# Optimization experiments

Hardware: AMD Instinct MI355X
Metric: run time of the kernel (lower is better)

Reference implementation:

```python
import jax, jax.numpy as jnp
import numpy as np

C, H, V, K, B, T = 1024, 256, 10000, 32, 8, 256
K1K = 2 * K + 1


def setup_inputs() -> dict:
    key = jax.random.key(0)
    ks = jax.random.split(key, 12)
    s = 0.05
    n = lambda k, shp: jax.random.normal(k, shp, dtype=jnp.float32) * s
    z = lambda shp: jnp.zeros(shp, dtype=jnp.float32)
    return {
        'text': jax.random.randint(ks[0], (B, T), 0, V, dtype=jnp.int32),
        'start_emb': n(ks[1], (H,)),
        'start_lin_W': n(ks[2], (H, H)), 'start_lin_b': z((H,)),
        'start_res_W1': n(ks[3], (2, H, H)), 'start_res_b1': z((2, H)),
        'start_res_W2': n(ks[4], (2, H, H)), 'start_res_b2': z((2, H)),
        'state_emb': n(ks[5], (C, H)),
        'next_state_emb': n(ks[6], (C, H)),
        'preterminal_emb': n(ks[7], (C, H)),
        'term_res_W1': n(ks[8], (2, H, H)), 'term_res_b1': z((2, H)),
        'term_res_W2': n(ks[9], (2, H, H)), 'term_res_b2': z((2, H)),
        'terminal_emb': n(ks[10], (V, H)),
        'col_banded_transition': n(ks[11], (C, K1K)),
    }


def _res(x, W1, b1, W2, b2):
    # ResLayer: x + ReLU(Linear(ReLU(Linear(x))))
    h = jax.nn.relu(x @ W1.T + b1)
    h = jax.nn.relu(h @ W2.T + b2)
    return x + h


def _band_to_dense(band):
    # BandedMatrix(band[None], K, K, fill=0).to_dense(): dense[i, i+d] = band[i, d+K] for |d|<=K
    offs = jnp.arange(-K, K + 1)                  # (K1K,)
    rows = jnp.arange(C)
    cols = rows[:, None] + offs[None, :]          # (C, K1K)
    valid = (cols >= 0) & (cols < C)
    vals = jnp.where(valid, band, 0.0)
    return jnp.zeros((C, C), band.dtype).at[rows[:, None], jnp.clip(cols, 0, C - 1)].add(vals)


def reference(text, start_emb, start_lin_W, start_lin_b,
              start_res_W1, start_res_b1, start_res_W2, start_res_b2,
              state_emb, next_state_emb, preterminal_emb,
              term_res_W1, term_res_b1, term_res_W2, term_res_b2,
              terminal_emb, col_banded_transition):
    # start(): MLP(start_emb) @ next_state_emb.T (tie_start), log_softmax -> (C,)
    fx = start_emb @ start_lin_W.T + start_lin_b
    for i in range(2):
        fx = _res(fx, start_res_W1[i], start_res_b1[i], start_res_W2[i], start_res_b2[i])
    start = jax.nn.log_softmax(fx @ next_state_emb.T)

    # transition(): dense logits + banded logits (band_method='product'), row log_softmax -> (C, C)
    logits = state_emb @ next_state_emb.T
    trans = jax.nn.log_softmax(logits + _band_to_dense(col_banded_transition), axis=-1)

    # emission(): terminal_mlp(preterminal_emb) @ terminal_emb.T, log_softmax -> (C, V)
    ft = preterminal_emb
    for i in range(2):
        ft = _res(ft, term_res_W1[i], term_res_b1[i], term_res_W2[i], term_res_b2[i])
    emit_T = jax.nn.log_softmax(ft @ terminal_emb.T, axis=-1).T  # (V, C)

    # HMM forward algorithm over time (log semiring)
    alpha = start[None, :] + emit_T[text[:, 0]]  # (B, C)

    def step(alpha, toks):
        # alpha_next[b, j] = logsumexp_i(alpha[b, i] + trans[i, j]) + emit[j, tok_b]
        a = jax.nn.logsumexp(alpha[:, :, None] + trans[None], axis=1) + emit_T[toks]
        return a, None

    alpha, _ = jax.lax.scan(step, alpha, text[:, 1:].T)
    return jax.nn.logsumexp(alpha, axis=-1)  # (B,) log-evidence
```

## Files before the change

### kernel.cpp

```cpp
#include <hip/hip_runtime.h>

constexpr int C = 1024, H = 256, V = 10000, K = 32, B = 8, T = 256, K1K = 65;
constexpr int DB = 32;
constexpr int GSCAN = B * DB;
constexpr float LV = 9.210340371976184f;

#define DEV static __device__ __forceinline__

typedef float f4 __attribute__((ext_vector_type(4)));

DEV void gstore(float* p, float v) {
  __hip_atomic_store((unsigned*)p, __float_as_uint(v), __ATOMIC_RELAXED, __HIP_MEMORY_SCOPE_AGENT);
}
DEV float gload(const float* p) {
  return __uint_as_float(__hip_atomic_load((unsigned*)p, __ATOMIC_RELAXED, __HIP_MEMORY_SCOPE_AGENT));
}
DEV void fstore(unsigned* p, unsigned v) {
  __hip_atomic_store(p, v, __ATOMIC_RELAXED, __HIP_MEMORY_SCOPE_AGENT);
}
DEV unsigned fload(const unsigned* p) {
  return __hip_atomic_load(p, __ATOMIC_RELAXED, __HIP_MEMORY_SCOPE_AGENT);
}

__global__ void __launch_bounds__(256) k_pre(
    const float* __restrict__ semb, const float* __restrict__ linW, const float* __restrict__ linb,
    const float* __restrict__ srW1, const float* __restrict__ srb1,
    const float* __restrict__ srW2, const float* __restrict__ srb2,
    const float* __restrict__ nse, const float* __restrict__ se,
    const float* __restrict__ pre, const float* __restrict__ trW1, const float* __restrict__ trb1,
    const float* __restrict__ trW2, const float* __restrict__ trb2,
    const float* __restrict__ band,
    unsigned* __restrict__ flags, float* __restrict__ startv,
    float* __restrict__ ft, float* __restrict__ PT) {
  __shared__ float smem[2048];
  const int bid = blockIdx.x, tid = threadIdx.x;

  if (bid == 0) {
    for (int k = tid; k < B * DB * 16; k += 256) flags[k] = 0u;
    return;
  }

  if (bid == 1) {
    float* sa = smem;
    float* fx = smem + 256;
    float* hh = smem + 512;
    float* sl = smem + 768;
    float* red = smem + 1792;
    sa[tid] = semb[tid];
    __syncthreads();
    float acc = linb[tid];
    for (int h = 0; h < H; ++h) acc += sa[h] * linW[tid * H + h];
    fx[tid] = acc;
    __syncthreads();
    for (int l = 0; l < 2; ++l) {
      float a1 = srb1[l * H + tid];
      const float* w1 = srW1 + (size_t)l * H * H + (size_t)tid * H;
      for (int h = 0; h < H; ++h) a1 += fx[h] * w1[h];
      hh[tid] = fmaxf(a1, 0.f);
      __syncthreads();
      float a2 = srb2[l * H + tid];
      const float* w2 = srW2 + (size_t)l * H * H + (size_t)tid * H;
      for (int h = 0; h < H; ++h) a2 += hh[h] * w2[h];
      __syncthreads();
      fx[tid] += fmaxf(a2, 0.f);
      __syncthreads();
    }
    for (int q = 0; q < 4; ++q) {
      int c = q * 256 + tid;
      const float* nr = nse + (size_t)c * H;
      float s = 0.f;
      for (int h = 0; h < H; ++h) s += fx[h] * nr[h];
      sl[c] = s;
    }
    __syncthreads();
    float m = -__builtin_inff();
    for (int q = 0; q < 4; ++q) m = fmaxf(m, sl[q * 256 + tid]);
    red[tid] = m; __syncthreads();
    for (int off = 128; off > 0; off >>= 1) { if (tid < off) red[tid] = fmaxf(red[tid], red[tid + off]); __syncthreads(); }
    m = red[0]; __syncthreads();
    float s = 0.f;
    for (int q = 0; q < 4; ++q) s += __expf(sl[q * 256 + tid] - m);
    red[tid] = s; __syncthreads();
    for (int off = 128; off > 0; off >>= 1) { if (tid < off) red[tid] += red[tid + off]; __syncthreads(); }
    float lse = m + __logf(red[0]);
    for (int q = 0; q < 4; ++q) { int c = q * 256 + tid; startv[c] = sl[c] - lse; }
    return;
  }

  if (bid < 258) {
    float (*x)[H] = (float(*)[H])smem;
    float (*hh)[H] = (float(*)[H])(smem + 1024);
    int r0 = (bid - 2) * 4;
    for (int r = 0; r < 4; ++r) x[r][tid] = pre[(size_t)(r0 + r) * H + tid];
    __syncthreads();
    for (int l = 0; l < 2; ++l) {
      float bb = trb1[l * H + tid];
      float a0 = bb, a1 = bb, a2 = bb, a3 = bb;
      const float* w1 = trW1 + (size_t)l * H * H + (size_t)tid * H;
      for (int h = 0; h < H; ++h) {
        float w = w1[h];
        a0 += x[0][h] * w; a1 += x[1][h] * w; a2 += x[2][h] * w; a3 += x[3][h] * w;
      }
      hh[0][tid] = fmaxf(a0, 0.f); hh[1][tid] = fmaxf(a1, 0.f);
      hh[2][tid] = fmaxf(a2, 0.f); hh[3][tid] = fmaxf(a3, 0.f);
      __syncthreads();
      bb = trb2[l * H + tid];
      float b0 = bb, b1 = bb, b2 = bb, b3 = bb;
      const float* w2 = trW2 + (size_t)l * H * H + (size_t)tid * H;
      for (int h = 0; h < H; ++h) {
        float w = w2[h];
        b0 += hh[0][h] * w; b1 += hh[1][h] * w; b2 += hh[2][h] * w; b3 += hh[3][h] * w;
      }
      __syncthreads();
      x[0][tid] += fmaxf(b0, 0.f); x[1][tid] += fmaxf(b1, 0.f);
      x[2][tid] += fmaxf(b2, 0.f); x[3][tid] += fmaxf(b3, 0.f);
      __syncthreads();
    }
    for (int r = 0; r < 4; ++r) ft[(size_t)(r0 + r) * H + tid] = x[r][tid];
    return;
  }

  {
    float* sv = smem;
    float* sl = smem + 256;
    float* rr = smem + 1280;
    int i = bid - 258;
    sv[tid] = se[(size_t)i * H + tid];
    __syncthreads();
    #pragma unroll 1
    for (int jq = 0; jq < 4; ++jq) {
      int j = jq * 256 + tid;
      const float4* nr = (const float4*)(nse + (size_t)j * H);
      float acc = 0.f;
      #pragma unroll 8
      for (int h4 = 0; h4 < H / 4; ++h4) {
        float4 nv = nr[h4];
        float4 s4 = *(const float4*)&sv[h4 * 4];
        acc += s4.x * nv.x + s4.y * nv.y + s4.z * nv.z + s4.w * nv.w;
      }
      sl[j] = acc;
    }
    __syncthreads();
    if (tid < K1K) {
      int col = i + tid - K;
      if (col >= 0 && col < C) sl[col] += band[(size_t)i * K1K + tid];
    }
    __syncthreads();
    float m = -__builtin_inff();
    for (int q = 0; q < 4; ++q) m = fmaxf(m, sl[q * 256 + tid]);
    rr[tid] = m; __syncthreads();
    for (int off = 128; off > 0; off >>= 1) { if (tid < off) rr[tid] = fmaxf(rr[tid], rr[tid + off]); __syncthreads(); }
    m = rr[0]; __syncthreads();
    float e[4]; float s = 0.f;
    for (int q = 0; q < 4; ++q) { e[q] = __expf(sl[q * 256 + tid] - m); s += e[q]; }
    rr[tid] = s; __syncthreads();
    for (int off = 128; off > 0; off >>= 1) { if (tid < off) rr[tid] += rr[tid + off]; __syncthreads(); }
    float inv = 1.f / rr[0];
    for (int q = 0; q < 4; ++q) {
      int j = q * 256 + tid;
      PT[(size_t)j * C + i] = e[q] * inv;
    }
  }
}

__global__ void __launch_bounds__(256) k_denom_part(
    const float* __restrict__ ft, const float* __restrict__ term, float* __restrict__ dpart) {
  constexpr int TJ = 16, VC = V / 8;
  __shared__ float shm[TJ * 4], shs[TJ * 4];
  int tid = threadIdx.x, lane = tid & 63, w = tid >> 6;
  int jg = blockIdx.x >> 3, vc = blockIdx.x & 7;
  const float4* fb = (const float4*)(ft + (size_t)jg * TJ * H);
  float rm[TJ], rs[TJ];
  #pragma unroll
  for (int r = 0; r < TJ; ++r) { rm[r] = -__builtin_inff(); rs[r] = 0.f; }
  int v0 = vc * VC;
  for (int v = v0 + tid; v < v0 + VC; v += 256) {
    const float4* tr = (const float4*)(term + (size_t)v * H);
    float acc[TJ];
    #pragma unroll
    for (int r = 0; r < TJ; ++r) acc[r] = 0.f;
    for (int h4 = 0; h4 < H / 4; ++h4) {
      float4 tv = tr[h4];
      #pragma unroll
      for (int r = 0; r < TJ; ++r) {
        float4 f = fb[r * (H / 4) + h4];
        acc[r] += tv.x * f.x + tv.y * f.y + tv.z * f.z + tv.w * f.w;
      }
    }
    #pragma unroll
    for (int r = 0; r < TJ; ++r) {
      float m2 = fmaxf(rm[r], acc[r]);
      rs[r] = rs[r] * __expf(rm[r] - m2) + __expf(acc[r] - m2);
      rm[r] = m2;
    }
  }
  #pragma unroll
  for (int r = 0; r < TJ; ++r) {
    float m = rm[r], s = rs[r];
    #pragma unroll
    for (int off = 32; off > 0; off >>= 1) {
      float mo = __shfl_xor(m, off), so = __shfl_xor(s, off);
      float m2 = fmaxf(m, mo);
      s = s * __expf(m - m2) + so * __expf(mo - m2);
      m = m2;
    }
    if (lane == 0) { shm[r * 4 + w] = m; shs[r * 4 + w] = s; }
  }
  __syncthreads();
  if (tid < TJ) {
    float m = -__builtin_inff(), s = 0.f;
    for (int w2 = 0; w2 < 4; ++w2) {
      float mo = shm[tid * 4 + w2], so = shs[tid * 4 + w2];
      float m2 = fmaxf(m, mo);
      s = s * __expf(m - m2) + so * __expf(mo - m2);
      m = m2;
    }
    int j = jg * TJ + tid;
    dpart[(j * 8 + vc) * 2 + 0] = m;
    dpart[(j * 8 + vc) * 2 + 1] = s;
  }
}

__global__ void k_denom_comb(const float* __restrict__ dpart, float* __restrict__ denom) {
  int j = blockIdx.x * 256 + threadIdx.x;
  float m = -__builtin_inff(), s = 0.f;
  for (int vc = 0; vc < 8; ++vc) {
    float mo = dpart[(j * 8 + vc) * 2], so = dpart[(j * 8 + vc) * 2 + 1];
    float m2 = fmaxf(m, mo);
    s = s * __expf(m - m2) + so * __expf(mo - m2);
    m = m2;
  }
  denom[j] = m + __logf(s);
}

__global__ void __launch_bounds__(256) k_eemit(
    const int* __restrict__ text, const float* __restrict__ ft,
    const float* __restrict__ denom, const float* __restrict__ term,
    float* __restrict__ eem) {
  int tid = threadIdx.x;
  int n0 = blockIdx.x * 8;
  const float4* trow[8];
  #pragma unroll
  for (int r = 0; r < 8; ++r) {
    int n = n0 + r;
    int tok = text[(n & 7) * T + (n >> 3)];
    trow[r] = (const float4*)(term + (size_t)tok * H);
  }
  for (int q = 0; q < 4; ++q) {
    int j = q * 256 + tid;
    const float4* fr = (const float4*)(ft + (size_t)j * H);
    float acc[8];
    #pragma unroll
    for (int r = 0; r < 8; ++r) acc[r] = 0.f;
    for (int h4 = 0; h4 < H / 4; ++h4) {
      float4 f = fr[h4];
      #pragma unroll
      for (int r = 0; r < 8; ++r) {
        float4 tv = trow[r][h4];
        acc[r] += f.x * tv.x + f.y * tv.y + f.z * tv.z + f.w * tv.w;
      }
    }
    float dj = denom[j];
    #pragma unroll
    for (int r = 0; r < 8; ++r) eem[(size_t)(n0 + r) * C + j] = __expf(acc[r] - dj + LV);
  }
}

__global__ void __launch_bounds__(256, 1) k_scan(
    const float* __restrict__ PT, const float* __restrict__ eem,
    const float* __restrict__ startv, float* __restrict__ pay,
    float* __restrict__ umax, unsigned* __restrict__ flags, float* __restrict__ out) {
  __shared__ __align__(16) float us[8 * 132];
  __shared__ float wv[32];
  __shared__ float fred[256];
  const int tid = threadIdx.x, bid = blockIdx.x;
  const int b = bid & 7, blk = bid >> 3;
  const int jbase = blk * 32;
  const int jloc = tid >> 3, s = tid & 7;
  const int myj = jbase + jloc;
  const bool owner = (s == 0);

  f4 pv[32];
  {
    const f4* prow = (const f4*)(PT + (size_t)myj * C + s * 128);
    #pragma unroll
    for (int k4 = 0; k4 < 32; ++k4) pv[k4] = prow[k4];
  }

  unsigned* myflag = &flags[(b * DB + blk) * 16];
  float Sacc = 0.f;

  if (owner) {
    float u0 = __expf(startv[myj]) * eem[(size_t)b * C + myj];
    gstore(&pay[(size_t)b * (DB * DB) + blk * DB + jloc], u0);
  }
  __syncthreads();
  if (tid == 0) fstore(myflag, 1u);

  float em = 0.f;
  if (owner) em = eem[((size_t)1 * B + b) * C + myj];

  for (int t = 1; t < T; ++t) {
    if (tid < DB) {
      while (fload(&flags[(b * DB + tid) * 16]) < (unsigned)t) {}
    }
    __syncthreads();

    float imt = 1.f;
    if (owner && (t & 7) == 1 && t > 1) {
      float m = gload(&umax[((t - 1) >> 3) * 8 + b]);
      imt = 1.f / m;
      Sacc += __logf(m);
    }

    {
      int i = (tid >> 3) * 32 + (tid & 7) * 4;
      const float* src = pay + (size_t)(((t - 1) & 1) * 8 + b) * (DB * DB) + i;
      f4 r;
      asm volatile("global_load_dwordx4 %0, %1, off sc0 sc1\n\ts_waitcnt vmcnt(0)"
                   : "=v"(r) : "v"(src) : "memory");
      int ph = (i >> 7) * 132 + (i & 127);
      *(f4*)&us[ph] = r;
    }
    __syncthreads();

    float acc = 0.f;
    {
      const int ubo = s * 132;
      #pragma unroll
      for (int k4 = 0; k4 < 32; ++k4) {
        f4 p = pv[k4];
        f4 x = *(const f4*)&us[ubo + k4 * 4];
        acc += p.x * x.x + p.y * x.y + p.z * x.z + p.w * x.w;
      }
    }
    acc += __shfl_xor(acc, 1);
    acc += __shfl_xor(acc, 2);
    acc += __shfl_xor(acc, 4);

    if (owner) {
      float val = acc * imt * em;
      gstore(&pay[(size_t)((t & 1) * 8 + b) * (DB * DB) + blk * DB + jloc], val);
      if (blk == 0) wv[jloc] = val;
    }
    __syncthreads();

    if (blk == 0 && (t & 7) == 0 && tid == 0) {
      float m = wv[0];
      #pragma unroll
      for (int j2 = 1; j2 < 32; ++j2) m = fmaxf(m, wv[j2]);
      gstore(&umax[(t >> 3) * 8 + b], m);
      asm volatile("s_waitcnt vmcnt(0)" ::: "memory");
    }
    if (tid == 0) fstore(myflag, (unsigned)(t + 1));
    if (owner && t + 1 < T) em = eem[((size_t)(t + 1) * B + b) * C + myj];
  }

  if (tid < DB) {
    while (fload(&flags[(b * DB + tid) * 16]) < (unsigned)T) {}
  }
  __syncthreads();
  if (blk == 0) {
    {
      int i = (tid >> 3) * 32 + (tid & 7) * 4;
      const float* src = pay + (size_t)(((T - 1) & 1) * 8 + b) * (DB * DB) + i;
      f4 r;
      asm volatile("global_load_dwordx4 %0, %1, off sc0 sc1\n\ts_waitcnt vmcnt(0)"
                   : "=v"(r) : "v"(src) : "memory");
      int ph = (i >> 7) * 132 + (i & 127);
      *(f4*)&us[ph] = r;
    }
    __syncthreads();
    float ss = 0.f;
    for (int idx = tid; idx < C; idx += 256) ss += us[(idx >> 7) * 132 + (idx & 127)];
    fred[tid] = ss;
    __syncthreads();
    for (int off = 128; off > 0; off >>= 1) {
      if (tid < off) fred[tid] += fred[tid + off];
      __syncthreads();
    }
    if (tid == 0) out[b] = -(float)T * LV + Sacc + __logf(fred[0]);
  }
}

extern "C" void kernel_launch(void* const* d_in, const int* in_sizes, int n_in,
                              void* d_out, int out_size, void* d_ws, size_t ws_size,
                              hipStream_t stream) {
  const int*   text  = (const int*)  d_in[0];
  const float* semb  = (const float*)d_in[1];
  const float* slinW = (const float*)d_in[2];
  const float* slinb = (const float*)d_in[3];
  const float* srW1  = (const float*)d_in[4];
  const float* srb1  = (const float*)d_in[5];
  const float* srW2  = (const float*)d_in[6];
  const float* srb2  = (const float*)d_in[7];
  const float* stemb = (const float*)d_in[8];
  const float* nse   = (const float*)d_in[9];
  const float* pre   = (const float*)d_in[10];
  const float* trW1  = (const float*)d_in[11];
  const float* trb1  = (const float*)d_in[12];
  const float* trW2  = (const float*)d_in[13];
  const float* trb2  = (const float*)d_in[14];
  const float* term  = (const float*)d_in[15];
  const float* band  = (const float*)d_in[16];

  float* ws     = (float*)d_ws;
  float* PT     = ws;
  float* eem    = PT + (size_t)C * C;
  float* pay    = eem + (size_t)T * B * C;
  float* ftb    = pay + 2 * 8 * DB * DB;
  float* startv = ftb + (size_t)C * H;
  float* denom  = startv + C;
  float* dpart  = denom + C;
  float* umax   = dpart + C * 16;
  unsigned* flags = (unsigned*)(umax + 32 * 8);

  k_pre<<<1282, 256, 0, stream>>>(semb, slinW, slinb, srW1, srb1, srW2, srb2,
                                  nse, stemb, pre, trW1, trb1, trW2, trb2, band,
                                  flags, startv, ftb, PT);
  k_denom_part<<<(C / 16) * 8, 256, 0, stream>>>(ftb, term, dpart);
  k_denom_comb<<<C / 256, 256, 0, stream>>>(dpart, denom);
  k_eemit<<<(T * B) / 8, 256, 0, stream>>>(text, ftb, denom, term, eem);
  k_scan<<<GSCAN, 256, 0, stream>>>(PT, eem, startv, pay, umax, flags, (float*)d_out);
}
```

Baseline: 969.4 us.

## Replace flag-based scan sync with sentinel-tagged payload polling and tune pre kernels

The cross-block HMM scan stops spinning on per-block flag counters. Each consumer now polls the payload buffer directly, which is 4-deep and pre-filled with a negative-sign sentinel, and producers reset slots two steps ahead. This removes a flag round-trip and one barrier per time step, at the risk of relying on alpha values never having the sign bit set. The terminal MLP inner loops are also vectorised with float4 accumulators, and the denominator kernel's row tile is doubled to 32.

```diff
diff --git a/kernel.cpp b/kernel.cpp
--- a/kernel.cpp
+++ b/kernel.cpp
@@ -4,6 +4,7 @@
 constexpr int DB = 32;
 constexpr int GSCAN = B * DB;
 constexpr float LV = 9.210340371976184f;
+constexpr unsigned SENT = 0x80000000u;
 
 #define DEV static __device__ __forceinline__
 
@@ -14,12 +15,6 @@
 }
 DEV float gload(const float* p) {
   return __uint_as_float(__hip_atomic_load((unsigned*)p, __ATOMIC_RELAXED, __HIP_MEMORY_SCOPE_AGENT));
-}
-DEV void fstore(unsigned* p, unsigned v) {
-  __hip_atomic_store(p, v, __ATOMIC_RELAXED, __HIP_MEMORY_SCOPE_AGENT);
-}
-DEV unsigned fload(const unsigned* p) {
-  return __hip_atomic_load(p, __ATOMIC_RELAXED, __HIP_MEMORY_SCOPE_AGENT);
 }
 
 __global__ void __launch_bounds__(256) k_pre(
@@ -30,17 +25,19 @@
     const float* __restrict__ pre, const float* __restrict__ trW1, const float* __restrict__ trb1,
     const float* __restrict__ trW2, const float* __restrict__ trb2,
     const float* __restrict__ band,
-    unsigned* __restrict__ flags, float* __restrict__ startv,
+    float* __restrict__ pay, float* __restrict__ startv,
     float* __restrict__ ft, float* __restrict__ PT) {
   __shared__ float smem[2048];
   const int bid = blockIdx.x, tid = threadIdx.x;
 
-  if (bid == 0) {
-    for (int k = tid; k < B * DB * 16; k += 256) flags[k] = 0u;
+  if (bid < 16) {
+    unsigned* p = (unsigned*)pay;
+    #pragma unroll
+    for (int k = 0; k < 8; ++k) p[bid * 2048 + k * 256 + tid] = SENT;
     return;
   }
 
-  if (bid == 1) {
+  if (bid == 16) {
     float* sa = smem;
     float* fx = smem + 256;
     float* hh = smem + 512;
@@ -87,33 +84,49 @@
     return;
   }
 
-  if (bid < 258) {
+  if (bid < 273) {
     float (*x)[H] = (float(*)[H])smem;
     float (*hh)[H] = (float(*)[H])(smem + 1024);
-    int r0 = (bid - 2) * 4;
+    int r0 = (bid - 17) * 4;
     for (int r = 0; r < 4; ++r) x[r][tid] = pre[(size_t)(r0 + r) * H + tid];
     __syncthreads();
     for (int l = 0; l < 2; ++l) {
-      float bb = trb1[l * H + tid];
-      float a0 = bb, a1 = bb, a2 = bb, a3 = bb;
-      const float* w1 = trW1 + (size_t)l * H * H + (size_t)tid * H;
-      for (int h = 0; h < H; ++h) {
-        float w = w1[h];
-        a0 += x[0][h] * w; a1 += x[1][h] * w; a2 += x[2][h] * w; a3 += x[3][h] * w;
-      }
-      hh[0][tid] = fmaxf(a0, 0.f); hh[1][tid] = fmaxf(a1, 0.f);
-      hh[2][tid] = fmaxf(a2, 0.f); hh[3][tid] = fmaxf(a3, 0.f);
-      __syncthreads();
-      bb = trb2[l * H + tid];
-      float b0 = bb, b1 = bb, b2 = bb, b3 = bb;
-      const float* w2 = trW2 + (size_t)l * H * H + (size_t)tid * H;
-      for (int h = 0; h < H; ++h) {
-        float w = w2[h];
-        b0 += hh[0][h] * w; b1 += hh[1][h] * w; b2 += hh[2][h] * w; b3 += hh[3][h] * w;
-      }
-      __syncthreads();
-      x[0][tid] += fmaxf(b0, 0.f); x[1][tid] += fmaxf(b1, 0.f);
-      x[2][tid] += fmaxf(b2, 0.f); x[3][tid] += fmaxf(b3, 0.f);
+      {
+        const f4* w1 = (const f4*)(trW1 + (size_t)l * H * H + (size_t)tid * H);
+        f4 p0 = {0.f, 0.f, 0.f, 0.f}, p1 = p0, p2 = p0, p3 = p0;
+        #pragma unroll 8
+        for (int h4 = 0; h4 < H / 4; ++h4) {
+          f4 w = w1[h4];
+          p0 += w * *(const f4*)&x[0][h4 * 4];
+          p1 += w * *(const f4*)&x[1][h4 * 4];
+          p2 += w * *(const f4*)&x[2][h4 * 4];
+          p3 += w * *(const f4*)&x[3][h4 * 4];
+        }
+        float bb = trb1[l * H + tid];
+        hh[0][tid] = fmaxf(p0.x + p0.y + p0.z + p0.w + bb, 0.f);
+        hh[1][tid] = fmaxf(p1.x + p1.y + p1.z + p1.w + bb, 0.f);
+        hh[2][tid] = fmaxf(p2.x + p2.y + p2.z + p2.w + bb, 0.f);
+        hh[3][tid] = fmaxf(p3.x + p3.y + p3.z + p3.w + bb, 0.f);
+      }
+      __syncthreads();
+      {
+        const f4* w2 = (const f4*)(trW2 + (size_t)l * H * H + (size_t)tid * H);
+        f4 q0 = {0.f, 0.f, 0.f, 0.f}, q1 = q0, q2 = q0, q3 = q0;
+        #pragma unroll 8
+        for (int h4 = 0; h4 < H / 4; ++h4) {
+          f4 w = w2[h4];
+          q0 += w * *(const f4*)&hh[0][h4 * 4];
+          q1 += w * *(const f4*)&hh[1][h4 * 4];
+          q2 += w * *(const f4*)&hh[2][h4 * 4];
+          q3 += w * *(const f4*)&hh[3][h4 * 4];
+        }
+        float bb = trb2[l * H + tid];
+        __syncthreads();
+        x[0][tid] += fmaxf(q0.x + q0.y + q0.z + q0.w + bb, 0.f);
+        x[1][tid] += fmaxf(q1.x + q1.y + q1.z + q1.w + bb, 0.f);
+        x[2][tid] += fmaxf(q2.x + q2.y + q2.z + q2.w + bb, 0.f);
+        x[3][tid] += fmaxf(q3.x + q3.y + q3.z + q3.w + bb, 0.f);
+      }
       __syncthreads();
     }
     for (int r = 0; r < 4; ++r) ft[(size_t)(r0 + r) * H + tid] = x[r][tid];
@@ -124,7 +137,7 @@
     float* sv = smem;
     float* sl = smem + 256;
     float* rr = smem + 1280;
-    int i = bid - 258;
+    int i = bid - 273;
     sv[tid] = se[(size_t)i * H + tid];
     __syncthreads();
     #pragma unroll 1
@@ -165,7 +178,7 @@
 
 __global__ void __launch_bounds__(256) k_denom_part(
     const float* __restrict__ ft, const float* __restrict__ term, float* __restrict__ dpart) {
-  constexpr int TJ = 16, VC = V / 8;
+  constexpr int TJ = 32, VC = V / 8;
   __shared__ float shm[TJ * 4], shs[TJ * 4];
   int tid = threadIdx.x, lane = tid & 63, w = tid >> 6;
   int jg = blockIdx.x >> 3, vc = blockIdx.x & 7;
@@ -269,15 +282,14 @@
 __global__ void __launch_bounds__(256, 1) k_scan(
     const float* __restrict__ PT, const float* __restrict__ eem,
     const float* __restrict__ startv, float* __restrict__ pay,
-    float* __restrict__ umax, unsigned* __restrict__ flags, float* __restrict__ out) {
+    float* __restrict__ umax, float* __restrict__ out) {
   __shared__ __align__(16) float us[8 * 132];
   __shared__ float wv[32];
   __shared__ float fred[256];
   const int tid = threadIdx.x, bid = blockIdx.x;
   const int b = bid & 7, blk = bid >> 3;
-  const int jbase = blk * 32;
   const int jloc = tid >> 3, s = tid & 7;
-  const int myj = jbase + jloc;
+  const int myj = blk * 32 + jloc;
   const bool owner = (s == 0);
 
   f4 pv[32];
@@ -285,26 +297,42 @@
     const f4* prow = (const f4*)(PT + (size_t)myj * C + s * 128);
     #pragma unroll
     for (int k4 = 0; k4 < 32; ++k4) pv[k4] = prow[k4];
-  }
-
-  unsigned* myflag = &flags[(b * DB + blk) * 16];
+    #pragma unroll
+    for (int k4 = 0; k4 < 32; ++k4) asm volatile("" : "+v"(pv[k4]));
+  }
+
   float Sacc = 0.f;
 
   if (owner) {
     float u0 = __expf(startv[myj]) * eem[(size_t)b * C + myj];
-    gstore(&pay[(size_t)b * (DB * DB) + blk * DB + jloc], u0);
-  }
-  __syncthreads();
-  if (tid == 0) fstore(myflag, 1u);
-
-  float em = 0.f;
-  if (owner) em = eem[((size_t)1 * B + b) * C + myj];
-
+    gstore(&pay[(size_t)b * C + myj], u0);
+  }
+  float em = owner ? eem[((size_t)B + b) * C + myj] : 0.f;
+
+  const int pi = tid * 4;
   for (int t = 1; t < T; ++t) {
-    if (tid < DB) {
-      while (fload(&flags[(b * DB + tid) * 16]) < (unsigned)t) {}
-    }
-    __syncthreads();
+    {
+      const float* src = pay + (size_t)((t - 1) & 3) * (B * C) + (size_t)b * C + pi;
+      f4 r;
+      for (;;) {
+        asm volatile("global_load_dwordx4 %0, %1, off sc0 sc1\n\ts_waitcnt vmcnt(0)"
+                     : "=v"(r) : "v"(src) : "memory");
+        unsigned bits = __float_as_uint(r.x) | __float_as_uint(r.y) |
+                        __float_as_uint(r.z) | __float_as_uint(r.w);
+        if (!(bits & 0x80000000u)) break;
+        __builtin_amdgcn_s_sleep(1);
+      }
+      int ph = (pi >> 7) * 132 + (pi & 127);
+      *(f4*)&us[ph] = r;
+    }
+    __syncthreads();
+
+    if (tid < 8) {
+      float* dst = pay + (size_t)((t + 1) & 3) * (B * C) + (size_t)b * C + blk * 32 + tid * 4;
+      f4 sn;
+      sn.x = sn.y = sn.z = sn.w = __uint_as_float(SENT);
+      asm volatile("global_store_dwordx4 %0, %1, off sc0 sc1" :: "v"(dst), "v"(sn) : "memory");
+    }
 
     float imt = 1.f;
     if (owner && (t & 7) == 1 && t > 1) {
@@ -312,17 +340,6 @@
       imt = 1.f / m;
       Sacc += __logf(m);
     }
-
-    {
-      int i = (tid >> 3) * 32 + (tid & 7) * 4;
-      const float* src = pay + (size_t)(((t - 1) & 1) * 8 + b) * (DB * DB) + i;
-      f4 r;
-      asm volatile("global_load_dwordx4 %0, %1, off sc0 sc1\n\ts_waitcnt vmcnt(0)"
-                   : "=v"(r) : "v"(src) : "memory");
-      int ph = (i >> 7) * 132 + (i & 127);
-      *(f4*)&us[ph] = r;
-    }
-    __syncthreads();
 
     float acc = 0.f;
     {
@@ -338,11 +355,12 @@
     acc += __shfl_xor(acc, 2);
     acc += __shfl_xor(acc, 4);
 
+    float val = 0.f;
     if (owner) {
-      float val = acc * imt * em;
-      gstore(&pay[(size_t)((t & 1) * 8 + b) * (DB * DB) + blk * DB + jloc], val);
+      val = acc * imt * em;
       if (blk == 0) wv[jloc] = val;
     }
+    if (tid < 8) asm volatile("s_waitcnt vmcnt(0)" ::: "memory");
     __syncthreads();
 
     if (blk == 0 && (t & 7) == 0 && tid == 0) {
@@ -352,28 +370,24 @@
       gstore(&umax[(t >> 3) * 8 + b], m);
       asm volatile("s_waitcnt vmcnt(0)" ::: "memory");
     }
-    if (tid == 0) fstore(myflag, (unsigned)(t + 1));
+    if (owner) gstore(&pay[(size_t)(t & 3) * (B * C) + (size_t)b * C + myj], val);
     if (owner && t + 1 < T) em = eem[((size_t)(t + 1) * B + b) * C + myj];
   }
 
-  if (tid < DB) {
-    while (fload(&flags[(b * DB + tid) * 16]) < (unsigned)T) {}
-  }
-  __syncthreads();
   if (blk == 0) {
     {
-      int i = (tid >> 3) * 32 + (tid & 7) * 4;
-      const float* src = pay + (size_t)(((T - 1) & 1) * 8 + b) * (DB * DB) + i;
+      const float* src = pay + (size_t)((T - 1) & 3) * (B * C) + (size_t)b * C + pi;
       f4 r;
-      asm volatile("global_load_dwordx4 %0, %1, off sc0 sc1\n\ts_waitcnt vmcnt(0)"
-                   : "=v"(r) : "v"(src) : "memory");
-      int ph = (i >> 7) * 132 + (i & 127);
-      *(f4*)&us[ph] = r;
-    }
-    __syncthreads();
-    float ss = 0.f;
-    for (int idx = tid; idx < C; idx += 256) ss += us[(idx >> 7) * 132 + (idx & 127)];
-    fred[tid] = ss;
+      for (;;) {
+        asm volatile("global_load_dwordx4 %0, %1, off sc0 sc1\n\ts_waitcnt vmcnt(0)"
+                     : "=v"(r) : "v"(src) : "memory");
+        unsigned bits = __float_as_uint(r.x) | __float_as_uint(r.y) |
+                        __float_as_uint(r.z) | __float_as_uint(r.w);
+        if (!(bits & 0x80000000u)) break;
+        __builtin_amdgcn_s_sleep(1);
+      }
+      fred[tid] = r.x + r.y + r.z + r.w;
+    }
     __syncthreads();
     for (int off = 128; off > 0; off >>= 1) {
       if (tid < off) fred[tid] += fred[tid + off];
@@ -408,18 +422,17 @@
   float* PT     = ws;
   float* eem    = PT + (size_t)C * C;
   float* pay    = eem + (size_t)T * B * C;
-  float* ftb    = pay + 2 * 8 * DB * DB;
+  float* ftb    = pay + 4 * B * C;
   float* startv = ftb + (size_t)C * H;
   float* denom  = startv + C;
   float* dpart  = denom + C;
   float* umax   = dpart + C * 16;
-  unsigned* flags = (unsigned*)(umax + 32 * 8);
-
-  k_pre<<<1282, 256, 0, stream>>>(semb, slinW, slinb, srW1, srb1, srW2, srb2,
+
+  k_pre<<<1297, 256, 0, stream>>>(semb, slinW, slinb, srW1, srb1, srW2, srb2,
                                   nse, stemb, pre, trW1, trb1, trW2, trb2, band,
-                                  flags, startv, ftb, PT);
-  k_denom_part<<<(C / 16) * 8, 256, 0, stream>>>(ftb, term, dpart);
+                                  pay, startv, ftb, PT);
+  k_denom_part<<<(C / 32) * 8, 256, 0, stream>>>(ftb, term, dpart);
   k_denom_comb<<<C / 256, 256, 0, stream>>>(dpart, denom);
   k_eemit<<<(T * B) / 8, 256, 0, stream>>>(text, ftb, denom, term, eem);
-  k_scan<<<GSCAN, 256, 0, stream>>>(PT, eem, startv, pay, umax, flags, (float*)d_out);
-}
+  k_scan<<<GSCAN, 256, 0, stream>>>(PT, eem, startv, pay, umax, (float*)d_out);
+}
```

Result: slower. 1.123 ms (+15.9%).
